# Optimization experiments

Hardware: AMD Instinct MI355X
Metric: run time of the kernel (lower is better)

## Reference

```python
import jax, jax.numpy as jnp
import numpy as np

N = 262144          # total points
C = 16              # classes
AVG_DEG = 16
E = N * AVG_DEG     # edges
LAMBDA1 = 0.7
LAMBDA2 = 0.5
LAMBDA_S = 0.2
LOSS_WEIGHT = 1.0
IGNORE_INDEX = -1
EPS = 1e-8


def setup_inputs() -> dict:
    key = jax.random.key(0)
    k1, k2, k3, k4 = jax.random.split(key, 4)
    pred = jax.random.normal(k1, (N, C), dtype=jnp.float32)
    target = jax.random.randint(k2, (N,), 0, C, dtype=jnp.int64)
    # precomputed radius-graph edge list (row = destination, col = source)
    row = jax.random.randint(k3, (E,), 0, N, dtype=jnp.int64)
    col = jax.random.randint(k4, (E,), 0, N, dtype=jnp.int64)
    return {"pred": pred, "target": target, "row": row, "col": col}


def _masked_mean(x, mask):
    cnt = jnp.sum(mask.astype(x.dtype))
    s = jnp.sum(jnp.where(mask, x, jnp.zeros_like(x)))
    return jnp.where(cnt > 0, s / jnp.maximum(cnt, 1.0), s)


def reference(pred, target, row, col):
    # per-point CE (reduction='none'); ignored points contribute 0
    log_probs = jax.nn.log_softmax(pred, axis=1)          # [N, C]
    probs = jnp.exp(log_probs)                            # [N, C]
    valid_mask = target != IGNORE_INDEX
    tgt = jnp.where(valid_mask, target, 0)
    ce_per_point = -jnp.take_along_axis(log_probs, tgt[:, None], axis=1)[:, 0]
    ce_per_point = jnp.where(valid_mask, ce_per_point, 0.0)

    conf = jnp.max(probs, axis=1)                         # [N]
    pred_label = jnp.argmax(probs, axis=1)                # [N]

    # degree per destination node
    deg = jax.ops.segment_sum(jnp.ones((E,), dtype=probs.dtype), row, num_segments=N)

    # neighborhood agreement u_i = mean_{j in N(i)} [pred_j == pred_i]
    agree_edge = (pred_label[col] == pred_label[row]).astype(probs.dtype)
    sum_agree = jax.ops.segment_sum(agree_edge, row, num_segments=N)
    u = jnp.where(deg > 0, sum_agree / jnp.maximum(deg, 1.0), jnp.ones_like(sum_agree))

    w = 1.0 + LAMBDA1 * (1.0 - u) + LAMBDA2 * (1.0 - conf)
    loss_ce = _masked_mean(w * ce_per_point, valid_mask)

    # per-edge KL(p_i || p_j) with clamp at 1e-8, scatter-mean over neighbors
    pi = probs[row]                                       # [E, C]
    pj = probs[col]                                       # [E, C]
    kl_edge = jnp.sum(
        pi * (jnp.log(jnp.maximum(pi, EPS)) - jnp.log(jnp.maximum(pj, EPS))), axis=1
    )                                                     # [E]
    sum_kl = jax.ops.segment_sum(kl_edge, row, num_segments=N)
    mean_kl = jnp.where(deg > 0, sum_kl / jnp.maximum(deg, 1.0), jnp.zeros_like(sum_kl))
    loss_smooth = _masked_mean(mean_kl, valid_mask)

    return (loss_ce + LAMBDA_S * loss_smooth) * LOSS_WEIGHT
```

## Files before the change

kernel.cpp:

```cpp
#include <hip/hip_runtime.h>

constexpr float LAMBDA1  = 0.7f;
constexpr float LAMBDA2  = 0.5f;
constexpr float LAMBDA_S = 0.2f;
constexpr float LOG_EPS  = -18.420680743952367f;
constexpr float PQ_SCALE  = 15.0f;
constexpr float LQ_SCALE4 = 15.0f / 18.420680743952367f;
constexpr float DOT_SCALE4 = 18.420680743952367f / (15.0f * 15.0f);

constexpr int      BUCK_SHIFT = 10;
constexpr unsigned BUCK_CAP   = 20480u;
constexpr int      CHUNK      = 8192;
constexpr int      BKT_THREADS = 1024;
constexpr int      CUR_PAD    = 16;
constexpr int      NB_NODE    = 256;

#if defined(__has_builtin)
#if __has_builtin(__builtin_amdgcn_udot8)
#define HAS_UDOT8 1
#endif
#endif

__global__ void k_point(const float* __restrict__ pred,
                        const int*   __restrict__ target,
                        unsigned long long* __restrict__ probsQ4,
                        unsigned long long* __restrict__ logpQ4,
                        float* __restrict__ Hn,
                        float* __restrict__ confn,
                        float* __restrict__ cen,
                        int n) {
    int i = blockIdx.x * blockDim.x + threadIdx.x;
    if (i >= n) return;

    const float4* p4 = reinterpret_cast<const float4*>(pred + (size_t)i * 16);
    float4 v0 = p4[0], v1 = p4[1], v2 = p4[2], v3 = p4[3];
    float x[16] = {v0.x, v0.y, v0.z, v0.w,
                   v1.x, v1.y, v1.z, v1.w,
                   v2.x, v2.y, v2.z, v2.w,
                   v3.x, v3.y, v3.z, v3.w};

    float m = x[0];
#pragma unroll
    for (int c = 1; c < 16; ++c) m = fmaxf(m, x[c]);

    float s = 0.f;
#pragma unroll
    for (int c = 0; c < 16; ++c) s += __expf(x[c] - m);
    float logZ = m + __logf(s);

    unsigned long long pq64 = 0ull, lq64 = 0ull;
    float Hacc = 0.f;
#pragma unroll
    for (int c = 0; c < 16; ++c) {
        float lp  = x[c] - logZ;
        float p   = __expf(lp);
        float lpc = fmaxf(lp, LOG_EPS);
        Hacc += p * lpc;

        unsigned pq = (unsigned)(int)rintf(p * PQ_SCALE);
        unsigned lq = (unsigned)(int)rintf(-lpc * LQ_SCALE4);
        pq64 |= (unsigned long long)pq << (4 * c);
        lq64 |= (unsigned long long)lq << (4 * c);
    }

    probsQ4[i] = pq64;
    logpQ4[i]  = lq64;

    Hn[i]    = Hacc;
    confn[i] = __expf(m - logZ);

    int t = target[i];
    bool valid = (t != -1);
    int tt = valid ? t : 0;
    float xt = x[0];
#pragma unroll
    for (int c = 1; c < 16; ++c) xt = (c == tt) ? x[c] : xt;
    cen[i] = valid ? -(xt - logZ) : 0.f;
}

__global__ void k_init(unsigned* __restrict__ gcursor) {
    int t = threadIdx.x;
    gcursor[t * CUR_PAD] = (unsigned)t * BUCK_CAP;
}

__global__ void __launch_bounds__(BKT_THREADS)
k_bucket(const int* __restrict__ row,
         const int* __restrict__ col,
         unsigned* __restrict__ bucketed,
         unsigned* __restrict__ gcursor,
         int e) {
    __shared__ unsigned stage[CHUNK];
    __shared__ unsigned char bid[CHUNK];
    __shared__ unsigned hist[256];
    __shared__ unsigned cnt[256];
    __shared__ unsigned lofs[256];
    __shared__ unsigned scanBuf[256];
    __shared__ unsigned baseArr[256];

    int t = threadIdx.x;
    if (t < 256) { hist[t] = 0; cnt[t] = 0; }
    __syncthreads();

    long i0 = (long)blockIdx.x * CHUNK;
    int chunkN = (int)(((long)e - i0) < CHUNK ? ((long)e - i0) : CHUNK);
    if (chunkN < 0) chunkN = 0;

    for (int k = t; k < chunkN; k += BKT_THREADS) {
        int r = __builtin_nontemporal_load(row + i0 + k);
        atomicAdd(&hist[r >> BUCK_SHIFT], 1u);
    }
    __syncthreads();

    if (t < 256) scanBuf[t] = hist[t];
    __syncthreads();
#pragma unroll
    for (int d = 1; d < 256; d <<= 1) {
        unsigned val = 0;
        if (t < 256 && t >= d) val = scanBuf[t - d];
        __syncthreads();
        if (t < 256) scanBuf[t] += val;
        __syncthreads();
    }
    if (t < 256) {
        lofs[t] = scanBuf[t] - hist[t];
        baseArr[t] = atomicAdd(&gcursor[t * CUR_PAD], hist[t]);
    }
    __syncthreads();

    for (int k = t; k < chunkN; k += BKT_THREADS) {
        int r = row[i0 + k];
        int c = __builtin_nontemporal_load(col + i0 + k);
        int b = r >> BUCK_SHIFT;
        unsigned s = lofs[b] + atomicAdd(&cnt[b], 1u);
        stage[s] = ((unsigned)(r & 1023) << 18) | (unsigned)c;
        bid[s]   = (unsigned char)b;
    }
    __syncthreads();

    for (int k = t; k < chunkN; k += BKT_THREADS) {
        unsigned b   = bid[k];
        unsigned dst = baseArr[b] + ((unsigned)k - lofs[b]);
        if (dst < (b + 1) * BUCK_CAP)
            bucketed[dst] = stage[k];
    }
}

__global__ void k_reduce(const unsigned* __restrict__ bucketed,
                         const unsigned* __restrict__ gcursor,
                         const unsigned long long* __restrict__ probsQ4,
                         const unsigned long long* __restrict__ logpQ4,
                         unsigned long long* __restrict__ accPart,
                         int n) {
    __shared__ unsigned long long acc[1024];
    __shared__ unsigned long long Ptab[1024];
    int t = threadIdx.x;
    int b = blockIdx.x >> 2;
    int q = blockIdx.x & 3;

    for (int i = t; i < 1024; i += 256) {
        acc[i] = 0ull;
        int node = (b << BUCK_SHIFT) + i;
        Ptab[i] = (node < n) ? probsQ4[node] : 0ull;
    }
    __syncthreads();

    unsigned nb = gcursor[b * CUR_PAD] - (unsigned)b * BUCK_CAP;
    if (nb > BUCK_CAP) nb = BUCK_CAP;
    unsigned s0 = (nb * (unsigned)q) >> 2;
    unsigned s1 = (nb * (unsigned)(q + 1)) >> 2;
    unsigned base = (unsigned)b * BUCK_CAP;

    for (unsigned k = s0 + (unsigned)t; k < s1; k += 256) {
        unsigned pl = bucketed[base + k];
        unsigned c  = pl & 0x3FFFFu;
        unsigned lr = pl >> 18;
        unsigned long long P = Ptab[lr];
        unsigned long long L = logpQ4[c];
        unsigned plo = (unsigned)P, phi = (unsigned)(P >> 32);
        unsigned llo = (unsigned)L, lhi = (unsigned)(L >> 32);

        unsigned dot;
#ifdef HAS_UDOT8
        dot = __builtin_amdgcn_udot8(plo, llo, 0u, false);
        dot = __builtin_amdgcn_udot8(phi, lhi, dot, false);
#else
        dot = 0;
#pragma unroll
        for (int k2 = 0; k2 < 8; ++k2) {
            dot += ((plo >> (4 * k2)) & 15u) * ((llo >> (4 * k2)) & 15u);
            dot += ((phi >> (4 * k2)) & 15u) * ((lhi >> (4 * k2)) & 15u);
        }
#endif
        int lab_r = 0, mr = -1;
#pragma unroll
        for (int k2 = 0; k2 < 8; ++k2) {
            int pv = (int)((plo >> (4 * k2)) & 15u);
            if (pv > mr) { mr = pv; lab_r = k2; }
        }
#pragma unroll
        for (int k2 = 0; k2 < 8; ++k2) {
            int pv = (int)((phi >> (4 * k2)) & 15u);
            if (pv > mr) { mr = pv; lab_r = 8 + k2; }
        }
        int lab_c = 0, mc = 1000;
#pragma unroll
        for (int k2 = 0; k2 < 8; ++k2) {
            int lv = (int)((llo >> (4 * k2)) & 15u);
            if (lv < mc) { mc = lv; lab_c = k2; }
        }
#pragma unroll
        for (int k2 = 0; k2 < 8; ++k2) {
            int lv = (int)((lhi >> (4 * k2)) & 15u);
            if (lv < mc) { mc = lv; lab_c = 8 + k2; }
        }

        unsigned long long add =
            ((unsigned long long)(0x10000u | (unsigned)(lab_r == lab_c)) << 32)
            | (unsigned long long)dot;
        atomicAdd(&acc[lr], add);
    }
    __syncthreads();

    for (int i = t; i < 1024; i += 256) {
        int node = (b << BUCK_SHIFT) + i;
        if (node < n) accPart[(size_t)q * n + node] = acc[i];
    }
}

__global__ void k_node(const int* __restrict__ target,
                       const float* __restrict__ confn,
                       const float* __restrict__ cen,
                       const float* __restrict__ Hn,
                       const unsigned long long* __restrict__ accPart,
                       float* __restrict__ partial,
                       int n) {
    float wce = 0.f, mkl = 0.f, v = 0.f;
    for (int i = blockIdx.x * blockDim.x + threadIdx.x; i < n;
         i += gridDim.x * blockDim.x) {
        unsigned long long pk = 0ull;
#pragma unroll
        for (int qx = 0; qx < 4; ++qx)
            pk += accPart[(size_t)qx * n + i];
        float deg  = (float)(unsigned)(pk >> 48);
        float sag  = (float)(unsigned)((pk >> 32) & 0xFFFFu);
        float sdot = (float)(unsigned)(pk & 0xFFFFFFFFull);
        float u  = (deg > 0.f) ? sag / deg : 1.f;
        float mk = (deg > 0.f) ? (Hn[i] + sdot * DOT_SCALE4 / deg) : 0.f;
        float w  = 1.f + LAMBDA1 * (1.f - u) + LAMBDA2 * (1.f - confn[i]);
        int t = target[i];
        if (t != -1) {
            wce += w * cen[i];
            mkl += mk;
            v   += 1.f;
        }
    }
#pragma unroll
    for (int off = 32; off > 0; off >>= 1) {
        wce += __shfl_down(wce, off, 64);
        mkl += __shfl_down(mkl, off, 64);
        v   += __shfl_down(v,   off, 64);
    }
    __shared__ float s[3][4];
    int wave = threadIdx.x >> 6, lane = threadIdx.x & 63;
    if (lane == 0) { s[0][wave] = wce; s[1][wave] = mkl; s[2][wave] = v; }
    __syncthreads();
    if (threadIdx.x == 0) {
        float a = 0.f, bb = 0.f, c = 0.f;
#pragma unroll
        for (int w = 0; w < 4; ++w) { a += s[0][w]; bb += s[1][w]; c += s[2][w]; }
        float4* p4 = reinterpret_cast<float4*>(partial);
        p4[blockIdx.x] = make_float4(a, bb, c, 0.f);
    }
}

__global__ void k_final(const float* __restrict__ partial, float* __restrict__ out) {
    int t = threadIdx.x;
    const float4* p4 = reinterpret_cast<const float4*>(partial);
    float4 pv = p4[t];
    float wce = pv.x, mkl = pv.y, v = pv.z;
#pragma unroll
    for (int off = 32; off > 0; off >>= 1) {
        wce += __shfl_down(wce, off, 64);
        mkl += __shfl_down(mkl, off, 64);
        v   += __shfl_down(v,   off, 64);
    }
    __shared__ float s[3][4];
    int wave = t >> 6, lane = t & 63;
    if (lane == 0) { s[0][wave] = wce; s[1][wave] = mkl; s[2][wave] = v; }
    __syncthreads();
    if (t == 0) {
        float a = 0.f, b = 0.f, c = 0.f;
#pragma unroll
        for (int w = 0; w < 4; ++w) { a += s[0][w]; b += s[1][w]; c += s[2][w]; }
        float lce = (c > 0.f) ? a / fmaxf(c, 1.f) : a;
        float ls  = (c > 0.f) ? b / fmaxf(c, 1.f) : b;
        out[0] = lce + LAMBDA_S * ls;
    }
}

extern "C" void kernel_launch(void* const* d_in, const int* in_sizes, int n_in,
                              void* d_out, int out_size, void* d_ws, size_t ws_size,
                              hipStream_t stream) {
    const float* pred   = (const float*)d_in[0];
    const int*   target = (const int*)d_in[1];
    const int*   row    = (const int*)d_in[2];
    const int*   col    = (const int*)d_in[3];
    float* out = (float*)d_out;

    const int n = in_sizes[1];
    const int e = in_sizes[2];

    const int nbuck = (n + 1023) >> BUCK_SHIFT;

    char* base = (char*)d_ws;
    size_t off = 0;
    unsigned long long* probsQ4 = (unsigned long long*)(base + off); off += (size_t)n * 8;
    unsigned long long* logpQ4  = (unsigned long long*)(base + off); off += (size_t)n * 8;
    float* Hn     = (float*)(base + off); off += (size_t)n * sizeof(float);
    float* confn  = (float*)(base + off); off += (size_t)n * sizeof(float);
    float* cen    = (float*)(base + off); off += (size_t)n * sizeof(float);
    unsigned* bucketed = (unsigned*)(base + off); off += (size_t)nbuck * BUCK_CAP * 4;
    unsigned* gcursor  = (unsigned*)(base + off); off += (size_t)nbuck * CUR_PAD * 4;
    unsigned long long* accPart = (unsigned long long*)(base + off); off += (size_t)4 * n * 8;
    float* partial = (float*)(base + off); off += (size_t)NB_NODE * 4 * sizeof(float);

    const int B = 256;
    k_point<<<(n + B - 1) / B, B, 0, stream>>>(pred, target, probsQ4, logpQ4,
                                               Hn, confn, cen, n);
    k_init<<<1, B, 0, stream>>>(gcursor);
    k_bucket<<<(e + CHUNK - 1) / CHUNK, BKT_THREADS, 0, stream>>>(row, col, bucketed,
                                                                  gcursor, e);
    k_reduce<<<nbuck * 4, B, 0, stream>>>(bucketed, gcursor, probsQ4, logpQ4,
                                          accPart, n);
    k_node<<<NB_NODE, B, 0, stream>>>(target, confn, cen, Hn,
                                      accPart, partial, n);
    k_final<<<1, B, 0, stream>>>(partial, out);
}
```

Measured before the change: 152.0 us.

## Fuse point and bucket kernels into one launch, precompute row labels

```diff
diff --git a/kernel.cpp b/kernel.cpp
--- a/kernel.cpp
+++ b/kernel.cpp
@@ -11,7 +11,7 @@
 constexpr int      BUCK_SHIFT = 10;
 constexpr unsigned BUCK_CAP   = 20480u;
 constexpr int      CHUNK      = 8192;
-constexpr int      BKT_THREADS = 1024;
+constexpr int      FT         = 1024;
 constexpr int      CUR_PAD    = 16;
 constexpr int      NB_NODE    = 256;
 
@@ -21,127 +21,131 @@
 #endif
 #endif
 
-__global__ void k_point(const float* __restrict__ pred,
-                        const int*   __restrict__ target,
-                        unsigned long long* __restrict__ probsQ4,
-                        unsigned long long* __restrict__ logpQ4,
-                        float* __restrict__ Hn,
-                        float* __restrict__ confn,
-                        float* __restrict__ cen,
-                        int n) {
-    int i = blockIdx.x * blockDim.x + threadIdx.x;
-    if (i >= n) return;
-
-    const float4* p4 = reinterpret_cast<const float4*>(pred + (size_t)i * 16);
-    float4 v0 = p4[0], v1 = p4[1], v2 = p4[2], v3 = p4[3];
-    float x[16] = {v0.x, v0.y, v0.z, v0.w,
-                   v1.x, v1.y, v1.z, v1.w,
-                   v2.x, v2.y, v2.z, v2.w,
-                   v3.x, v3.y, v3.z, v3.w};
-
-    float m = x[0];
-#pragma unroll
-    for (int c = 1; c < 16; ++c) m = fmaxf(m, x[c]);
-
-    float s = 0.f;
-#pragma unroll
-    for (int c = 0; c < 16; ++c) s += __expf(x[c] - m);
-    float logZ = m + __logf(s);
-
-    unsigned long long pq64 = 0ull, lq64 = 0ull;
-    float Hacc = 0.f;
-#pragma unroll
-    for (int c = 0; c < 16; ++c) {
-        float lp  = x[c] - logZ;
-        float p   = __expf(lp);
-        float lpc = fmaxf(lp, LOG_EPS);
-        Hacc += p * lpc;
-
-        unsigned pq = (unsigned)(int)rintf(p * PQ_SCALE);
-        unsigned lq = (unsigned)(int)rintf(-lpc * LQ_SCALE4);
-        pq64 |= (unsigned long long)pq << (4 * c);
-        lq64 |= (unsigned long long)lq << (4 * c);
-    }
-
-    probsQ4[i] = pq64;
-    logpQ4[i]  = lq64;
-
-    Hn[i]    = Hacc;
-    confn[i] = __expf(m - logZ);
-
-    int t = target[i];
-    bool valid = (t != -1);
-    int tt = valid ? t : 0;
-    float xt = x[0];
-#pragma unroll
-    for (int c = 1; c < 16; ++c) xt = (c == tt) ? x[c] : xt;
-    cen[i] = valid ? -(xt - logZ) : 0.f;
-}
-
-__global__ void k_init(unsigned* __restrict__ gcursor) {
+__global__ void __launch_bounds__(FT, 8)
+k_fused(const float* __restrict__ pred,
+        const int*   __restrict__ target,
+        unsigned long long* __restrict__ probsQ4,
+        unsigned long long* __restrict__ logpQ4,
+        float* __restrict__ Hn,
+        float* __restrict__ confn,
+        float* __restrict__ cen,
+        const int* __restrict__ row,
+        const int* __restrict__ col,
+        unsigned* __restrict__ bucketed,
+        unsigned* __restrict__ gcursor,
+        int n, int e, int bucketBlocks) {
     int t = threadIdx.x;
-    gcursor[t * CUR_PAD] = (unsigned)t * BUCK_CAP;
-}
-
-__global__ void __launch_bounds__(BKT_THREADS)
-k_bucket(const int* __restrict__ row,
-         const int* __restrict__ col,
-         unsigned* __restrict__ bucketed,
-         unsigned* __restrict__ gcursor,
-         int e) {
-    __shared__ unsigned stage[CHUNK];
-    __shared__ unsigned char bid[CHUNK];
-    __shared__ unsigned hist[256];
-    __shared__ unsigned cnt[256];
-    __shared__ unsigned lofs[256];
-    __shared__ unsigned scanBuf[256];
-    __shared__ unsigned baseArr[256];
-
-    int t = threadIdx.x;
-    if (t < 256) { hist[t] = 0; cnt[t] = 0; }
-    __syncthreads();
-
-    long i0 = (long)blockIdx.x * CHUNK;
-    int chunkN = (int)(((long)e - i0) < CHUNK ? ((long)e - i0) : CHUNK);
-    if (chunkN < 0) chunkN = 0;
-
-    for (int k = t; k < chunkN; k += BKT_THREADS) {
-        int r = __builtin_nontemporal_load(row + i0 + k);
-        atomicAdd(&hist[r >> BUCK_SHIFT], 1u);
-    }
-    __syncthreads();
-
-    if (t < 256) scanBuf[t] = hist[t];
-    __syncthreads();
-#pragma unroll
-    for (int d = 1; d < 256; d <<= 1) {
-        unsigned val = 0;
-        if (t < 256 && t >= d) val = scanBuf[t - d];
+
+    if ((int)blockIdx.x < bucketBlocks) {
+        __shared__ unsigned stage[CHUNK];
+        __shared__ unsigned char bid[CHUNK];
+        __shared__ unsigned hist[256];
+        __shared__ unsigned cnt[256];
+        __shared__ unsigned lofs[256];
+        __shared__ unsigned baseArr[256];
+
+        if (t < 256) { hist[t] = 0; cnt[t] = 0; }
         __syncthreads();
-        if (t < 256) scanBuf[t] += val;
+
+        long i0 = (long)blockIdx.x * CHUNK;
+        int chunkN = (int)(((long)e - i0) < CHUNK ? ((long)e - i0) : CHUNK);
+        if (chunkN < 0) chunkN = 0;
+
+        for (int k = t; k < chunkN; k += FT) {
+            int r = __builtin_nontemporal_load(row + i0 + k);
+            atomicAdd(&hist[r >> BUCK_SHIFT], 1u);
+        }
         __syncthreads();
-    }
-    if (t < 256) {
-        lofs[t] = scanBuf[t] - hist[t];
-        baseArr[t] = atomicAdd(&gcursor[t * CUR_PAD], hist[t]);
-    }
-    __syncthreads();
-
-    for (int k = t; k < chunkN; k += BKT_THREADS) {
-        int r = row[i0 + k];
-        int c = __builtin_nontemporal_load(col + i0 + k);
-        int b = r >> BUCK_SHIFT;
-        unsigned s = lofs[b] + atomicAdd(&cnt[b], 1u);
-        stage[s] = ((unsigned)(r & 1023) << 18) | (unsigned)c;
-        bid[s]   = (unsigned char)b;
-    }
-    __syncthreads();
-
-    for (int k = t; k < chunkN; k += BKT_THREADS) {
-        unsigned b   = bid[k];
-        unsigned dst = baseArr[b] + ((unsigned)k - lofs[b]);
-        if (dst < (b + 1) * BUCK_CAP)
-            bucketed[dst] = stage[k];
+
+        if (t < 64) {
+            unsigned h0 = hist[4 * t], h1 = hist[4 * t + 1],
+                     h2 = hist[4 * t + 2], h3 = hist[4 * t + 3];
+            unsigned s = h0 + h1 + h2 + h3;
+            unsigned inc = s;
+#pragma unroll
+            for (int off = 1; off < 64; off <<= 1) {
+                unsigned v = __shfl_up(inc, off, 64);
+                if (t >= off) inc += v;
+            }
+            unsigned run = inc - s;
+            lofs[4 * t]     = run;
+            lofs[4 * t + 1] = run + h0;
+            lofs[4 * t + 2] = run + h0 + h1;
+            lofs[4 * t + 3] = run + h0 + h1 + h2;
+#pragma unroll
+            for (int j = 0; j < 4; ++j) {
+                int b = 4 * t + j;
+                unsigned h = hist[b];
+                baseArr[b] = (unsigned)b * BUCK_CAP
+                           + atomicAdd(&gcursor[b * CUR_PAD], h);
+            }
+        }
+        __syncthreads();
+
+        for (int k = t; k < chunkN; k += FT) {
+            int r = row[i0 + k];
+            int c = __builtin_nontemporal_load(col + i0 + k);
+            int b = r >> BUCK_SHIFT;
+            unsigned s = lofs[b] + atomicAdd(&cnt[b], 1u);
+            stage[s] = ((unsigned)(r & 1023) << 18) | (unsigned)c;
+            bid[s]   = (unsigned char)b;
+        }
+        __syncthreads();
+
+        for (int k = t; k < chunkN; k += FT) {
+            unsigned b   = bid[k];
+            unsigned dst = baseArr[b] + ((unsigned)k - lofs[b]);
+            if (dst < (b + 1) * BUCK_CAP)
+                bucketed[dst] = stage[k];
+        }
+    } else {
+        int i = (blockIdx.x - bucketBlocks) * FT + t;
+        if (i >= n) return;
+
+        const float4* p4 = reinterpret_cast<const float4*>(pred + (size_t)i * 16);
+        float4 v0 = p4[0], v1 = p4[1], v2 = p4[2], v3 = p4[3];
+        float x[16] = {v0.x, v0.y, v0.z, v0.w,
+                       v1.x, v1.y, v1.z, v1.w,
+                       v2.x, v2.y, v2.z, v2.w,
+                       v3.x, v3.y, v3.z, v3.w};
+
+        float m = x[0];
+#pragma unroll
+        for (int c = 1; c < 16; ++c) m = fmaxf(m, x[c]);
+
+        float s = 0.f;
+#pragma unroll
+        for (int c = 0; c < 16; ++c) s += __expf(x[c] - m);
+        float logZ = m + __logf(s);
+
+        unsigned long long pq64 = 0ull, lq64 = 0ull;
+        float Hacc = 0.f;
+#pragma unroll
+        for (int c = 0; c < 16; ++c) {
+            float lp  = x[c] - logZ;
+            float p   = __expf(lp);
+            float lpc = fmaxf(lp, LOG_EPS);
+            Hacc += p * lpc;
+
+            unsigned pq = (unsigned)(int)rintf(p * PQ_SCALE);
+            unsigned lq = (unsigned)(int)rintf(-lpc * LQ_SCALE4);
+            pq64 |= (unsigned long long)pq << (4 * c);
+            lq64 |= (unsigned long long)lq << (4 * c);
+        }
+
+        probsQ4[i] = pq64;
+        logpQ4[i]  = lq64;
+
+        Hn[i]    = Hacc;
+        confn[i] = __expf(m - logZ);
+
+        int tt0 = target[i];
+        bool valid = (tt0 != -1);
+        int tt = valid ? tt0 : 0;
+        float xt = x[0];
+#pragma unroll
+        for (int c = 1; c < 16; ++c) xt = (c == tt) ? x[c] : xt;
+        cen[i] = valid ? -(xt - logZ) : 0.f;
     }
 }
 
@@ -153,6 +157,7 @@
                          int n) {
     __shared__ unsigned long long acc[1024];
     __shared__ unsigned long long Ptab[1024];
+    __shared__ unsigned char labr[1024];
     int t = threadIdx.x;
     int b = blockIdx.x >> 2;
     int q = blockIdx.x & 3;
@@ -160,11 +165,25 @@
     for (int i = t; i < 1024; i += 256) {
         acc[i] = 0ull;
         int node = (b << BUCK_SHIFT) + i;
-        Ptab[i] = (node < n) ? probsQ4[node] : 0ull;
+        unsigned long long P = (node < n) ? probsQ4[node] : 0ull;
+        Ptab[i] = P;
+        unsigned plo = (unsigned)P, phi = (unsigned)(P >> 32);
+        int lr = 0, mr = -1;
+#pragma unroll
+        for (int k2 = 0; k2 < 8; ++k2) {
+            int pv = (int)((plo >> (4 * k2)) & 15u);
+            if (pv > mr) { mr = pv; lr = k2; }
+        }
+#pragma unroll
+        for (int k2 = 0; k2 < 8; ++k2) {
+            int pv = (int)((phi >> (4 * k2)) & 15u);
+            if (pv > mr) { mr = pv; lr = 8 + k2; }
+        }
+        labr[i] = (unsigned char)lr;
     }
     __syncthreads();
 
-    unsigned nb = gcursor[b * CUR_PAD] - (unsigned)b * BUCK_CAP;
+    unsigned nb = gcursor[b * CUR_PAD];
     if (nb > BUCK_CAP) nb = BUCK_CAP;
     unsigned s0 = (nb * (unsigned)q) >> 2;
     unsigned s1 = (nb * (unsigned)(q + 1)) >> 2;
@@ -191,17 +210,6 @@
             dot += ((phi >> (4 * k2)) & 15u) * ((lhi >> (4 * k2)) & 15u);
         }
 #endif
-        int lab_r = 0, mr = -1;
-#pragma unroll
-        for (int k2 = 0; k2 < 8; ++k2) {
-            int pv = (int)((plo >> (4 * k2)) & 15u);
-            if (pv > mr) { mr = pv; lab_r = k2; }
-        }
-#pragma unroll
-        for (int k2 = 0; k2 < 8; ++k2) {
-            int pv = (int)((phi >> (4 * k2)) & 15u);
-            if (pv > mr) { mr = pv; lab_r = 8 + k2; }
-        }
         int lab_c = 0, mc = 1000;
 #pragma unroll
         for (int k2 = 0; k2 < 8; ++k2) {
@@ -214,8 +222,9 @@
             if (lv < mc) { mc = lv; lab_c = 8 + k2; }
         }
 
+        unsigned agree = ((int)labr[lr] == lab_c) ? 1u : 0u;
         unsigned long long add =
-            ((unsigned long long)(0x10000u | (unsigned)(lab_r == lab_c)) << 32)
+            ((unsigned long long)(0x10000u | agree) << 32)
             | (unsigned long long)dot;
         atomicAdd(&acc[lr], add);
     }
@@ -311,6 +320,8 @@
     const int e = in_sizes[2];
 
     const int nbuck = (n + 1023) >> BUCK_SHIFT;
+    const int bucketBlocks = (e + CHUNK - 1) / CHUNK;
+    const int pointBlocks  = (n + FT - 1) / FT;
 
     char* base = (char*)d_ws;
     size_t off = 0;
@@ -324,12 +335,12 @@
     unsigned long long* accPart = (unsigned long long*)(base + off); off += (size_t)4 * n * 8;
     float* partial = (float*)(base + off); off += (size_t)NB_NODE * 4 * sizeof(float);
 
+    hipMemsetAsync(gcursor, 0, (size_t)nbuck * CUR_PAD * 4, stream);
+
     const int B = 256;
-    k_point<<<(n + B - 1) / B, B, 0, stream>>>(pred, target, probsQ4, logpQ4,
-                                               Hn, confn, cen, n);
-    k_init<<<1, B, 0, stream>>>(gcursor);
-    k_bucket<<<(e + CHUNK - 1) / CHUNK, BKT_THREADS, 0, stream>>>(row, col, bucketed,
-                                                                  gcursor, e);
+    k_fused<<<bucketBlocks + pointBlocks, FT, 0, stream>>>(
+        pred, target, probsQ4, logpQ4, Hn, confn, cen,
+        row, col, bucketed, gcursor, n, e, bucketBlocks);
     k_reduce<<<nbuck * 4, B, 0, stream>>>(bucketed, gcursor, probsQ4, logpQ4,
                                           accPart, n);
     k_node<<<NB_NODE, B, 0, stream>>>(target, confn, cen, Hn,
```

New measurement: 150.4 us. About the same (-1.1%).
